# Performance work log

Hardware: AMD Instinct MI355X
Metric: run time of the kernel (lower is better)

## Reference

```python
import jax, jax.numpy as jnp
import numpy as np

B, S, D, H = 2, 2048, 1024, 16
DK = D // H

def setup_inputs() -> dict:
    key = jax.random.key(0)
    ks = jax.random.split(key, 11)
    s = 1.0 / np.sqrt(D)
    inp = {
        'q': jax.random.normal(ks[0], (B, S, D), jnp.float32),
        'k': jax.random.normal(ks[1], (B, S, D), jnp.float32),
        'v': jax.random.normal(ks[2], (B, S, D), jnp.float32),
        'mask': jnp.tril(jnp.ones((S, S), jnp.bool_))[None, None],  # [1,1,S,S] causal
        'w_q': jax.random.normal(ks[3], (D, D), jnp.float32) * s,
        'b_q': jax.random.normal(ks[4], (D,), jnp.float32) * s,
        'w_k': jax.random.normal(ks[5], (D, D), jnp.float32) * s,
        'b_k': jax.random.normal(ks[6], (D,), jnp.float32) * s,
        'w_v': jax.random.normal(ks[7], (D, D), jnp.float32) * s,
        'b_v': jax.random.normal(ks[8], (D,), jnp.float32) * s,
        'w_o': jax.random.normal(ks[9], (D, D), jnp.float32) * s,
        'b_o': jax.random.normal(ks[10], (D,), jnp.float32) * s,
    }
    return inp

def reference(q, k, v, mask, w_q, b_q, w_k, b_k, w_v, b_v, w_o, b_o):
    # Linear projections (torch Linear: x @ W^T + b)
    qh = (q @ w_q.T + b_q).reshape(B, S, H, DK).transpose(0, 2, 1, 3)  # [B,H,S,DK]
    kh = (k @ w_k.T + b_k).reshape(B, S, H, DK).transpose(0, 2, 1, 3)
    vh = (v @ w_v.T + b_v).reshape(B, S, H, DK).transpose(0, 2, 1, 3)
    scores = jnp.einsum('bhqd,bhkd->bhqk', qh, kh) / jnp.sqrt(jnp.float32(DK))
    scores = jnp.where(mask, scores, jnp.float32(-jnp.inf))
    attn = jax.nn.softmax(scores, axis=-1)  # dropout p=0.0 -> identity
    out = jnp.einsum('bhqk,bhkd->bhqd', attn, vh)
    out = out.transpose(0, 2, 1, 3).reshape(B, S, D)
    return out @ w_o.T + b_o
```

## Files before the change

kernel.cpp:

```cpp
#include <hip/hip_runtime.h>
#include <hip/hip_bf16.h>

typedef __bf16 bf16_t;
typedef __bf16 bf16x4 __attribute__((ext_vector_type(4)));
typedef __bf16 bf16x8 __attribute__((ext_vector_type(8)));
typedef float f32x4 __attribute__((ext_vector_type(4)));

#define B_ 2
#define S_ 2048
#define D_ 1024
#define H_ 16
#define DK_ 64
#define M_ (B_ * S_)

__device__ __forceinline__ f32x4 mfma16(bf16x8 a, bf16x8 b, f32x4 c) {
  return __builtin_amdgcn_mfma_f32_16x16x32_bf16(a, b, c, 0, 0, 0);
}

__device__ __forceinline__ void async_load16(const bf16_t* g, bf16_t* l) {
  __builtin_amdgcn_global_load_lds(
      (const __attribute__((address_space(1))) void*)g,
      (__attribute__((address_space(3))) void*)l, 16, 0, 0);
}


__global__ void cvt_all(const float* __restrict__ q, const float* __restrict__ k,
                        const float* __restrict__ v, const float* __restrict__ w0,
                        const float* __restrict__ w1, const float* __restrict__ w2,
                        const float* __restrict__ w3, bf16_t* __restrict__ qb,
                        bf16_t* __restrict__ kb, bf16_t* __restrict__ vb,
                        bf16_t* __restrict__ o0, bf16_t* __restrict__ o1,
                        bf16_t* __restrict__ o2, bf16_t* __restrict__ o3) {
  const int y = blockIdx.y;
  if (y >= 3 && blockIdx.x >= 512) return;
  const float* src;
  bf16_t* dst;
  float sc = 1.0f;
  switch (y) {
    case 0: src = q; dst = qb; break;
    case 1: src = k; dst = kb; break;
    case 2: src = v; dst = vb; break;
    case 3: src = w0; dst = o0; sc = 0.125f; break;
    case 4: src = w1; dst = o1; break;
    case 5: src = w2; dst = o2; break;
    default: src = w3; dst = o3; break;
  }
  long i = ((long)blockIdx.x * blockDim.x + threadIdx.x) * 8;
  const float4* s4 = (const float4*)(src + i);
  float4 a = s4[0], b = s4[1];
  bf16x8 o;
  o[0] = (bf16_t)(a.x * sc); o[1] = (bf16_t)(a.y * sc);
  o[2] = (bf16_t)(a.z * sc); o[3] = (bf16_t)(a.w * sc);
  o[4] = (bf16_t)(b.x * sc); o[5] = (bf16_t)(b.y * sc);
  o[6] = (bf16_t)(b.z * sc); o[7] = (bf16_t)(b.w * sc);
  *(bf16x8*)(dst + i) = o;
}


__device__ __forceinline__ int swzG(int b) {
  return b ^ (((b >> 7) & 7) << 4);
}

template <int NR>
__device__ __forceinline__ void stage_tile(const bf16_t* g, bf16_t* lds,
                                           const int* srcoff, int wave) {
#pragma unroll
  for (int rnd = 0; rnd < NR; ++rnd)
    async_load16(g + srcoff[rnd], lds + rnd * 2048 + wave * 512);
}

template <int MODE>
__device__ __forceinline__ void gemm_core8(const bf16_t* __restrict__ A,
                                           const bf16_t* __restrict__ W,
                                           const float* __restrict__ bias,
                                           float bscale, void* __restrict__ Cv,
                                           bf16_t* __restrict__ As,
                                           bf16_t* __restrict__ Bs) {
  constexpr int N = 1024, K = 1024;
  constexpr int TILE = 128 * 32;
  constexpr int NIT = K / 32;
  const int tid = threadIdx.x;
  const int wave = tid >> 6, lane = tid & 63;
  const int quad = lane >> 4, l15 = lane & 15;
  const int wm = wave >> 2, wn = wave & 3;
  const int bm = blockIdx.x * 128, bn = blockIdx.y * 128;

  f32x4 acc[4][2] = {};

  const int sb = swzG(tid * 16);
  const int srcoff = (sb >> 6) * K + ((sb & 63) >> 1);
  const bf16_t* ag = A + (long)bm * K;
  const bf16_t* bg = W + (long)bn * K;
  bf16_t* const adst = As;
  bf16_t* const bdst = Bs;

  const int xorv = ((l15 >> 1) & 7) << 4;
  const int aco = (((wm * 64 + l15) * 64 + quad * 16) ^ xorv) >> 1;
  const int bco = (((wn * 32 + l15) * 64 + quad * 16) ^ xorv) >> 1;

  async_load16(ag + srcoff, adst + wave * 512);
  async_load16(bg + srcoff, bdst + wave * 512);
  async_load16(ag + 32 + srcoff, adst + TILE + wave * 512);
  async_load16(bg + 32 + srcoff, bdst + TILE + wave * 512);

  int rb = 0, sb2 = 2;
  for (int j = 0; j < NIT; ++j) {
    if (j < NIT - 1)
      asm volatile("s_waitcnt vmcnt(2)" ::: "memory");
    else
      asm volatile("s_waitcnt vmcnt(0)" ::: "memory");
    __builtin_amdgcn_sched_barrier(0);
    __builtin_amdgcn_s_barrier();
    __builtin_amdgcn_sched_barrier(0);

    if (j + 2 < NIT) {
      const int kk2 = (j + 2) * 32;
      async_load16(ag + kk2 + srcoff, adst + sb2 * TILE + wave * 512);
      async_load16(bg + kk2 + srcoff, bdst + sb2 * TILE + wave * 512);
    }
    sb2 = (sb2 == 2) ? 0 : sb2 + 1;

    const bf16_t* Ac = As + rb * TILE;
    const bf16_t* Bc = Bs + rb * TILE;
    rb = (rb == 2) ? 0 : rb + 1;
    bf16x8 af[4], bfr[2];
#pragma unroll
    for (int i = 0; i < 4; ++i)
      af[i] = *(const bf16x8*)&Ac[aco + i * 512];
#pragma unroll
    for (int i = 0; i < 2; ++i)
      bfr[i] = *(const bf16x8*)&Bc[bco + i * 512];
    __builtin_amdgcn_s_setprio(1);
#pragma unroll
    for (int mi = 0; mi < 4; ++mi)
#pragma unroll
      for (int ni = 0; ni < 2; ++ni)
        acc[mi][ni] = mfma16(af[mi], bfr[ni], acc[mi][ni]);
    __builtin_amdgcn_s_setprio(0);
  }

#pragma unroll
  for (int mi = 0; mi < 4; ++mi) {
#pragma unroll
    for (int ni = 0; ni < 2; ++ni) {
      const int col = bn + wn * 32 + ni * 16 + l15;
      const float bsv = bias[col] * bscale;
      f32x4 v = acc[mi][ni];
      const int row0 = bm + wm * 64 + mi * 16 + quad * 4;
      if (MODE == 3) {
        float* C = (float*)Cv;
#pragma unroll
        for (int r = 0; r < 4; ++r)
          C[(long)(row0 + r) * N + col] = v[r] + bsv;
      } else if (MODE == 1) {
        bf16_t* C = (bf16_t*)Cv;
        const int hh = col >> 6, dk = col & 63;
        const int bq = row0 >> 11, s0 = row0 & 2047;
        bf16_t* base = C + (((long)bq * H_ + hh) * S_ + s0) * DK_ + dk;
#pragma unroll
        for (int r = 0; r < 4; ++r)
          base[(long)r * DK_] = (bf16_t)(v[r] + bsv);
      } else {
        bf16_t* C = (bf16_t*)Cv;
        const int hh = col >> 6, dk = col & 63;
        const int bq = row0 >> 11, s0 = row0 & 2047;
        bf16x4 pk;
#pragma unroll
        for (int r = 0; r < 4; ++r) pk[r] = (bf16_t)(v[r] + bsv);
        *(bf16x4*)(C + (((long)bq * H_ + hh) * DK_ + dk) * S_ + s0) = pk;
      }
    }
  }
}

__global__ __launch_bounds__(512) void gemm_qkv(
    const bf16_t* __restrict__ qb, const bf16_t* __restrict__ kb,
    const bf16_t* __restrict__ vb, const bf16_t* __restrict__ wq,
    const bf16_t* __restrict__ wk, const bf16_t* __restrict__ wv,
    const float* __restrict__ biq, const float* __restrict__ bik,
    const float* __restrict__ biv, bf16_t* __restrict__ Qh,
    bf16_t* __restrict__ Kh, bf16_t* __restrict__ Vt) {
  __shared__ bf16_t As[3][128 * 32];
  __shared__ bf16_t Bs[3][128 * 32];
  if (blockIdx.z == 0)
    gemm_core8<1>(qb, wq, biq, 0.125f, Qh, &As[0][0], &Bs[0][0]);
  else if (blockIdx.z == 1)
    gemm_core8<1>(kb, wk, bik, 1.0f, Kh, &As[0][0], &Bs[0][0]);
  else
    gemm_core8<2>(vb, wv, biv, 1.0f, Vt, &As[0][0], &Bs[0][0]);
}


__device__ __forceinline__ int swzG128(int b) {
  return b ^ (((b >> 7) & 7) << 4);
}

__global__ __launch_bounds__(256) void gemm_out64(
    const bf16_t* __restrict__ AO, const bf16_t* __restrict__ wo,
    const float* __restrict__ bo, float* __restrict__ out) {
  constexpr int N = 1024, K = 1024;
  constexpr int ATILE = 64 * 64, BTILE = 128 * 64;
  constexpr int NIT = K / 64;
  __shared__ bf16_t As[3][ATILE];
  __shared__ bf16_t Bs[3][BTILE];
  const int tid = threadIdx.x;
  const int wave = tid >> 6, lane = tid & 63;
  const int quad = lane >> 4, l15 = lane & 15;
  const int wm = wave >> 1, wn = wave & 1;
  const int bm = blockIdx.x * 64, bn = blockIdx.y * 128;

  f32x4 acc[2][4] = {};

  int srcoff[4];
#pragma unroll
  for (int rnd = 0; rnd < 4; ++rnd) {
    const int bb = rnd * 4096 + tid * 16;
    const int sb = swzG128(bb);
    srcoff[rnd] = (sb >> 7) * K + ((sb & 127) >> 1);
  }
  const bf16_t* ag = AO + (long)bm * K;
  const bf16_t* bg = wo + (long)bn * K;

  const int co0 = ((quad * 16) ^ ((l15 & 7) << 4)) >> 1;
  const int co1 = ((quad * 16 + 64) ^ ((l15 & 7) << 4)) >> 1;
  const int arow0 = (wm * 32 + l15) * 64;
  const int brow0 = (wn * 64 + l15) * 64;

  stage_tile<2>(ag, &As[0][0], srcoff, wave);
  stage_tile<4>(bg, &Bs[0][0], srcoff, wave);
  stage_tile<2>(ag + 64, &As[1][0], srcoff, wave);
  stage_tile<4>(bg + 64, &Bs[1][0], srcoff, wave);

  int rb = 0, sb2 = 2;
  for (int j = 0; j < NIT; ++j) {
    if (j < NIT - 1)
      asm volatile("s_waitcnt vmcnt(6)" ::: "memory");
    else
      asm volatile("s_waitcnt vmcnt(0)" ::: "memory");
    __builtin_amdgcn_sched_barrier(0);
    __builtin_amdgcn_s_barrier();
    __builtin_amdgcn_sched_barrier(0);

    if (j + 2 < NIT) {
      const int kk2 = (j + 2) * 64;
      stage_tile<2>(ag + kk2, &As[sb2][0], srcoff, wave);
      stage_tile<4>(bg + kk2, &Bs[sb2][0], srcoff, wave);
    }
    sb2 = (sb2 == 2) ? 0 : sb2 + 1;

    const bf16_t* Ac = &As[rb][0];
    const bf16_t* Bc = &Bs[rb][0];
    rb = (rb == 2) ? 0 : rb + 1;
#pragma unroll
    for (int h = 0; h < 2; ++h) {
      const int co = h ? co1 : co0;
      bf16x8 af[2], bfr[4];
#pragma unroll
      for (int i = 0; i < 2; ++i)
        af[i] = *(const bf16x8*)&Ac[arow0 + i * 1024 + co];
#pragma unroll
      for (int i = 0; i < 4; ++i)
        bfr[i] = *(const bf16x8*)&Bc[brow0 + i * 1024 + co];
      __builtin_amdgcn_s_setprio(1);
#pragma unroll
      for (int mi = 0; mi < 2; ++mi)
#pragma unroll
        for (int ni = 0; ni < 4; ++ni)
          acc[mi][ni] = mfma16(af[mi], bfr[ni], acc[mi][ni]);
      __builtin_amdgcn_s_setprio(0);
    }
  }

#pragma unroll
  for (int mi = 0; mi < 2; ++mi) {
#pragma unroll
    for (int ni = 0; ni < 4; ++ni) {
      const int col = bn + wn * 64 + ni * 16 + l15;
      const float bsv = bo[col];
      f32x4 v = acc[mi][ni];
      const int row0 = bm + wm * 32 + mi * 16 + quad * 4;
#pragma unroll
      for (int r = 0; r < 4; ++r)
        out[(long)(row0 + r) * N + col] = v[r] + bsv;
    }
  }
}


__device__ __forceinline__ int swzK(int b) {
  return b ^ (((b >> 7) & 3) << 4) ^ (((b >> 10) & 1) << 6);
}
__device__ __forceinline__ int swzV(int b) {
  return b ^ (((b >> 7) & 7) << 4);
}

template <bool MASKED>
__device__ __forceinline__ void softmax_pa(const f32x4 st[4], float& l_i,
                                           bf16x8& pa0, bf16x8& pa1,
                                           const int qcol, const int quad) {
#pragma unroll
  for (int nb = 0; nb < 4; ++nb) {
    const int kvb = quad * 8 + (nb & 1) * 4 + (nb >> 1) * 32;
#pragma unroll
    for (int r = 0; r < 4; ++r) {
      float x = st[nb][r];
      if (MASKED && (kvb + r) > qcol) x = -30000.f;
      const float pv = __expf(x);
      l_i += pv;
      const bf16_t pb = (bf16_t)pv;
      const int idx = ((nb & 1) << 2) | r;
      if (nb < 2) pa0[idx] = pb;
      else        pa1[idx] = pb;
    }
  }
}

__global__ __launch_bounds__(256, 2) void flash_attn3(
    const bf16_t* __restrict__ Qh, const bf16_t* __restrict__ Kh,
    const bf16_t* __restrict__ Vt, bf16_t* __restrict__ AO) {
  const int bid = blockIdx.x;
  const int g = bid & 31;
  const int i = bid >> 5;
  const int h = g & 15, b = g >> 4;
  const int tA = i, tB = 31 - i;
  const int tid = threadIdx.x, wave = tid >> 6, lane = tid & 63;
  const int quad = lane >> 4, l15 = lane & 15;
  const int qcol = wave * 16 + l15;
  const int prow = ((l15 >> 2) << 3) | (l15 & 3);

  __shared__ bf16_t Kls[3][64 * 64];
  __shared__ bf16_t Vls[3][64 * 64];

  const bf16_t* qhead = Qh + ((long)(b * H_ + h) * S_) * DK_;
  const bf16_t* khead = Kh + ((long)(b * H_ + h) * S_) * DK_;
  const bf16_t* vhead = Vt + ((long)(b * H_ + h) * DK_) * S_;

  int koffe[2], voffe[2], ldse[2];
#pragma unroll
  for (int c = 0; c < 2; ++c) {
    const int bb = c * 4096 + wave * 1024 + lane * 16;
    koffe[c] = swzK(bb) >> 1;
    const int vs = swzV(bb);
    voffe[c] = (vs >> 7) * S_ + ((vs & 127) >> 1);
    ldse[c] = c * 2048 + wave * 512;
  }

  int kro[4][2], vro[4][2];
#pragma unroll
  for (int nb = 0; nb < 4; ++nb) {
    const int krow = prow + (nb & 1) * 4 + (nb >> 1) * 32;
    const int vrow = nb * 16 + l15;
#pragma unroll
    for (int hh = 0; hh < 2; ++hh) {
      kro[nb][hh] = swzK(krow * 128 + quad * 16 + hh * 64) >> 1;
      vro[nb][hh] = swzV(vrow * 128 + quad * 16 + hh * 64) >> 1;
    }
  }

  const int qA = tA * 64 + wave * 16;
  const int qB = tB * 64 + wave * 16;
  const bf16_t* qpA = qhead + (long)(qA + l15) * DK_ + quad * 8;
  const bf16_t* qpB = qhead + (long)(qB + l15) * DK_ + quad * 8;
  const bf16x8 aqA0 = *(const bf16x8*)qpA;
  const bf16x8 aqA1 = *(const bf16x8*)(qpA + 32);
  const bf16x8 aqB0 = *(const bf16x8*)qpB;
  const bf16x8 aqB1 = *(const bf16x8*)(qpB + 32);

  f32x4 oA[4] = {}, oB[4] = {};
  float lA = 0.f, lB = 0.f;

#pragma unroll
  for (int c = 0; c < 2; ++c) {
    async_load16(khead + koffe[c], &Kls[0][ldse[c]]);
    async_load16(vhead + voffe[c], &Vls[0][ldse[c]]);
  }
#pragma unroll
  for (int c = 0; c < 2; ++c) {
    async_load16(khead + 64 * DK_ + koffe[c], &Kls[1][ldse[c]]);
    async_load16(vhead + 64 + voffe[c], &Vls[1][ldse[c]]);
  }

  int bi = 0;
  for (int j = 0; j <= tB; ++j) {
    if (j < tB)
      asm volatile("s_waitcnt vmcnt(4)" ::: "memory");
    else
      asm volatile("s_waitcnt vmcnt(0)" ::: "memory");
    __builtin_amdgcn_sched_barrier(0);
    __builtin_amdgcn_s_barrier();
    __builtin_amdgcn_sched_barrier(0);

    if (j + 2 <= tB) {
      const int tb2 = (bi == 0) ? 2 : (bi - 1);
      const bf16_t* kt = khead + (j + 2) * (64 * DK_);
      const bf16_t* vt = vhead + (j + 2) * 64;
#pragma unroll
      for (int c = 0; c < 2; ++c) {
        async_load16(kt + koffe[c], &Kls[tb2][ldse[c]]);
        async_load16(vt + voffe[c], &Vls[tb2][ldse[c]]);
      }
    }
    __builtin_amdgcn_sched_barrier(0);

    const bf16_t* Kc = &Kls[bi][0];
    const bf16_t* Vc = &Vls[bi][0];

    bf16x8 k0[4], k1[4];
#pragma unroll
    for (int nb = 0; nb < 4; ++nb) {
      k0[nb] = *(const bf16x8*)&Kc[kro[nb][0]];
      k1[nb] = *(const bf16x8*)&Kc[kro[nb][1]];
    }

    bf16x8 paB0, paB1, paA0, paA1;
    {
      f32x4 stB[4];
#pragma unroll
      for (int nb = 0; nb < 4; ++nb) {
        f32x4 t = {};
        t = mfma16(k0[nb], aqB0, t);
        t = mfma16(k1[nb], aqB1, t);
        stB[nb] = t;
      }
      if (j == tB)
        softmax_pa<true>(stB, lB, paB0, paB1, qcol, quad);
      else
        softmax_pa<false>(stB, lB, paB0, paB1, qcol, quad);
    }
    const bool doA = (j <= tA);
    if (doA) {
      f32x4 stA[4];
#pragma unroll
      for (int nb = 0; nb < 4; ++nb) {
        f32x4 t = {};
        t = mfma16(k0[nb], aqA0, t);
        t = mfma16(k1[nb], aqA1, t);
        stA[nb] = t;
      }
      if (j == tA)
        softmax_pa<true>(stA, lA, paA0, paA1, qcol, quad);
      else
        softmax_pa<false>(stA, lA, paA0, paA1, qcol, quad);
    }

    bf16x8 v0[4], v1[4];
#pragma unroll
    for (int nb = 0; nb < 4; ++nb) {
      v0[nb] = *(const bf16x8*)&Vc[vro[nb][0]];
      v1[nb] = *(const bf16x8*)&Vc[vro[nb][1]];
    }
#pragma unroll
    for (int nb = 0; nb < 4; ++nb) {
      oB[nb] = mfma16(paB0, v0[nb], oB[nb]);
      oB[nb] = mfma16(paB1, v1[nb], oB[nb]);
    }
    if (doA) {
#pragma unroll
      for (int nb = 0; nb < 4; ++nb) {
        oA[nb] = mfma16(paA0, v0[nb], oA[nb]);
        oA[nb] = mfma16(paA1, v1[nb], oA[nb]);
      }
    }

    bi = (bi == 2) ? 0 : bi + 1;
  }

  lA += __shfl_xor(lA, 16, 64);
  lA += __shfl_xor(lA, 32, 64);
  lB += __shfl_xor(lB, 16, 64);
  lB += __shfl_xor(lB, 32, 64);

  bf16_t* aoA = AO + (long)(b * S_ + qA + quad * 4) * D_ + h * DK_ + l15;
  bf16_t* aoB = AO + (long)(b * S_ + qB + quad * 4) * D_ + h * DK_ + l15;
#pragma unroll
  for (int r = 0; r < 4; ++r) {
    const float invA = 1.0f / __shfl(lA, quad * 4 + r, 64);
    const float invB = 1.0f / __shfl(lB, quad * 4 + r, 64);
#pragma unroll
    for (int nb = 0; nb < 4; ++nb) {
      aoA[(long)r * D_ + nb * 16] = (bf16_t)(oA[nb][r] * invA);
      aoB[(long)r * D_ + nb * 16] = (bf16_t)(oB[nb][r] * invB);
    }
  }
}


extern "C" void kernel_launch(void* const* d_in, const int* in_sizes, int n_in,
                              void* d_out, int out_size, void* d_ws, size_t ws_size,
                              hipStream_t stream) {
  const float* q = (const float*)d_in[0];
  const float* k = (const float*)d_in[1];
  const float* v = (const float*)d_in[2];
  const float* wq = (const float*)d_in[4];
  const float* bq = (const float*)d_in[5];
  const float* wk = (const float*)d_in[6];
  const float* bk = (const float*)d_in[7];
  const float* wv = (const float*)d_in[8];
  const float* bv = (const float*)d_in[9];
  const float* wo = (const float*)d_in[10];
  const float* bo = (const float*)d_in[11];
  float* out = (float*)d_out;

  char* ws = (char*)d_ws;
  const size_t MB = 1024 * 1024;
  bf16_t* Qh = (bf16_t*)(ws);
  bf16_t* Kh = (bf16_t*)(ws + 8 * MB);
  bf16_t* Vt = (bf16_t*)(ws + 16 * MB);
  bf16_t* AO = (bf16_t*)(ws + 24 * MB);
  bf16_t* qb = (bf16_t*)(ws + 32 * MB);
  bf16_t* kb = (bf16_t*)(ws + 40 * MB);
  bf16_t* vb = (bf16_t*)(ws + 48 * MB);
  bf16_t* wqb = (bf16_t*)(ws + 56 * MB);
  bf16_t* wkb = (bf16_t*)(ws + 58 * MB);
  bf16_t* wvb = (bf16_t*)(ws + 60 * MB);
  bf16_t* wob = (bf16_t*)(ws + 62 * MB);

  cvt_all<<<dim3(2048, 7, 1), 256, 0, stream>>>(q, k, v, wq, wk, wv, wo, qb, kb,
                                                vb, wqb, wkb, wvb, wob);
  gemm_qkv<<<dim3(32, 8, 3), 512, 0, stream>>>(qb, kb, vb, wqb, wkb, wvb, bq, bk,
                                               bv, Qh, Kh, Vt);
  flash_attn3<<<dim3(512, 1, 1), 256, 0, stream>>>(Qh, Kh, Vt, AO);
  gemm_out64<<<dim3(64, 8, 1), 256, 0, stream>>>(AO, wob, bo, out);
}
```

Measured before the change: 208.7 us.

## Fuse fp32-to-bf16 activation conversion into QKV projection GEMM loads

The separate pass that converted q, k and v from fp32 to bf16 is removed. The QKV GEMM now loads fp32 activation tiles into registers, converts them to bf16 and writes them to LDS itself, while the weight tiles still use async global-to-LDS loads. This drops the write and re-read of 3x8MB bf16 intermediates and shrinks the conversion kernel to weights only. In exchange, the GEMM fetches twice the A bytes, B fetches are re-read across 8 N-blocks, and the pipeline adds extra waitcnt stalls with register-staged A loads.

Result: slower. 238.7 us (+14.4%).

```diff
diff --git a/kernel.cpp b/kernel.cpp
--- a/kernel.cpp
+++ b/kernel.cpp
@@ -24,25 +24,18 @@
 }
 
 
-__global__ void cvt_all(const float* __restrict__ q, const float* __restrict__ k,
-                        const float* __restrict__ v, const float* __restrict__ w0,
-                        const float* __restrict__ w1, const float* __restrict__ w2,
-                        const float* __restrict__ w3, bf16_t* __restrict__ qb,
-                        bf16_t* __restrict__ kb, bf16_t* __restrict__ vb,
-                        bf16_t* __restrict__ o0, bf16_t* __restrict__ o1,
-                        bf16_t* __restrict__ o2, bf16_t* __restrict__ o3) {
+__global__ void cvt_w(const float* __restrict__ w0, const float* __restrict__ w1,
+                      const float* __restrict__ w2, const float* __restrict__ w3,
+                      bf16_t* __restrict__ o0, bf16_t* __restrict__ o1,
+                      bf16_t* __restrict__ o2, bf16_t* __restrict__ o3) {
   const int y = blockIdx.y;
-  if (y >= 3 && blockIdx.x >= 512) return;
   const float* src;
   bf16_t* dst;
   float sc = 1.0f;
   switch (y) {
-    case 0: src = q; dst = qb; break;
-    case 1: src = k; dst = kb; break;
-    case 2: src = v; dst = vb; break;
-    case 3: src = w0; dst = o0; sc = 0.125f; break;
-    case 4: src = w1; dst = o1; break;
-    case 5: src = w2; dst = o2; break;
+    case 0: src = w0; dst = o0; sc = 0.125f; break;
+    case 1: src = w1; dst = o1; break;
+    case 2: src = w2; dst = o2; break;
     default: src = w3; dst = o3; break;
   }
   long i = ((long)blockIdx.x * blockDim.x + threadIdx.x) * 8;
@@ -70,12 +63,12 @@
 }
 
 template <int MODE>
-__device__ __forceinline__ void gemm_core8(const bf16_t* __restrict__ A,
-                                           const bf16_t* __restrict__ W,
-                                           const float* __restrict__ bias,
-                                           float bscale, void* __restrict__ Cv,
-                                           bf16_t* __restrict__ As,
-                                           bf16_t* __restrict__ Bs) {
+__device__ __forceinline__ void gemm_core8f(const float* __restrict__ A,
+                                            const bf16_t* __restrict__ W,
+                                            const float* __restrict__ bias,
+                                            float bscale, void* __restrict__ Cv,
+                                            bf16_t* __restrict__ As,
+                                            bf16_t* __restrict__ Bs) {
   constexpr int N = 1024, K = 1024;
   constexpr int TILE = 128 * 32;
   constexpr int NIT = K / 32;
@@ -87,38 +80,58 @@
 
   f32x4 acc[4][2] = {};
 
-  const int sb = swzG(tid * 16);
-  const int srcoff = (sb >> 6) * K + ((sb & 63) >> 1);
-  const bf16_t* ag = A + (long)bm * K;
+  const int sbB = swzG(tid * 16);
+  const int bsrcoff = (sbB >> 6) * K + ((sbB & 63) >> 1);
   const bf16_t* bg = W + (long)bn * K;
-  bf16_t* const adst = As;
-  bf16_t* const bdst = Bs;
+
+  const int arow = tid >> 2;
+  const int acolf = (tid & 3) * 8;
+  const int awr = swzG(tid * 16) >> 1;
+  const float* agf = A + (long)(bm + arow) * K + acolf;
+
+  float4 aA_, aB_;
+  auto issueA = [&](int t) {
+    const float4* p = (const float4*)(agf + t * 32);
+    aA_ = p[0];
+    aB_ = p[1];
+  };
+  auto mathWriteA = [&](bf16_t* dstbuf) {
+    bf16x8 y;
+    y[0] = (bf16_t)aA_.x; y[1] = (bf16_t)aA_.y;
+    y[2] = (bf16_t)aA_.z; y[3] = (bf16_t)aA_.w;
+    y[4] = (bf16_t)aB_.x; y[5] = (bf16_t)aB_.y;
+    y[6] = (bf16_t)aB_.z; y[7] = (bf16_t)aB_.w;
+    *(bf16x8*)(dstbuf + awr) = y;
+  };
 
   const int xorv = ((l15 >> 1) & 7) << 4;
   const int aco = (((wm * 64 + l15) * 64 + quad * 16) ^ xorv) >> 1;
   const int bco = (((wn * 32 + l15) * 64 + quad * 16) ^ xorv) >> 1;
 
-  async_load16(ag + srcoff, adst + wave * 512);
-  async_load16(bg + srcoff, bdst + wave * 512);
-  async_load16(ag + 32 + srcoff, adst + TILE + wave * 512);
-  async_load16(bg + 32 + srcoff, bdst + TILE + wave * 512);
+  issueA(0);
+  async_load16(bg + bsrcoff, Bs + wave * 512);
+  mathWriteA(As);
+  issueA(1);
+  async_load16(bg + 32 + bsrcoff, Bs + TILE + wave * 512);
 
   int rb = 0, sb2 = 2;
   for (int j = 0; j < NIT; ++j) {
+    if (j + 1 < NIT) mathWriteA(As + ((j + 1) % 3) * TILE);
     if (j < NIT - 1)
-      asm volatile("s_waitcnt vmcnt(2)" ::: "memory");
+      asm volatile("s_waitcnt vmcnt(1)" ::: "memory");
     else
       asm volatile("s_waitcnt vmcnt(0)" ::: "memory");
+    asm volatile("s_waitcnt lgkmcnt(0)" ::: "memory");
     __builtin_amdgcn_sched_barrier(0);
     __builtin_amdgcn_s_barrier();
     __builtin_amdgcn_sched_barrier(0);
 
     if (j + 2 < NIT) {
-      const int kk2 = (j + 2) * 32;
-      async_load16(ag + kk2 + srcoff, adst + sb2 * TILE + wave * 512);
-      async_load16(bg + kk2 + srcoff, bdst + sb2 * TILE + wave * 512);
+      issueA(j + 2);
+      async_load16(bg + (j + 2) * 32 + bsrcoff, Bs + sb2 * TILE + wave * 512);
     }
     sb2 = (sb2 == 2) ? 0 : sb2 + 1;
+    __builtin_amdgcn_sched_barrier(0);
 
     const bf16_t* Ac = As + rb * TILE;
     const bf16_t* Bc = Bs + rb * TILE;
@@ -147,12 +160,7 @@
       const float bsv = bias[col] * bscale;
       f32x4 v = acc[mi][ni];
       const int row0 = bm + wm * 64 + mi * 16 + quad * 4;
-      if (MODE == 3) {
-        float* C = (float*)Cv;
-#pragma unroll
-        for (int r = 0; r < 4; ++r)
-          C[(long)(row0 + r) * N + col] = v[r] + bsv;
-      } else if (MODE == 1) {
+      if (MODE == 1) {
         bf16_t* C = (bf16_t*)Cv;
         const int hh = col >> 6, dk = col & 63;
         const int bq = row0 >> 11, s0 = row0 & 2047;
@@ -174,8 +182,8 @@
 }
 
 __global__ __launch_bounds__(512) void gemm_qkv(
-    const bf16_t* __restrict__ qb, const bf16_t* __restrict__ kb,
-    const bf16_t* __restrict__ vb, const bf16_t* __restrict__ wq,
+    const float* __restrict__ qf, const float* __restrict__ kf,
+    const float* __restrict__ vf, const bf16_t* __restrict__ wq,
     const bf16_t* __restrict__ wk, const bf16_t* __restrict__ wv,
     const float* __restrict__ biq, const float* __restrict__ bik,
     const float* __restrict__ biv, bf16_t* __restrict__ Qh,
@@ -183,11 +191,11 @@
   __shared__ bf16_t As[3][128 * 32];
   __shared__ bf16_t Bs[3][128 * 32];
   if (blockIdx.z == 0)
-    gemm_core8<1>(qb, wq, biq, 0.125f, Qh, &As[0][0], &Bs[0][0]);
+    gemm_core8f<1>(qf, wq, biq, 0.125f, Qh, &As[0][0], &Bs[0][0]);
   else if (blockIdx.z == 1)
-    gemm_core8<1>(kb, wk, bik, 1.0f, Kh, &As[0][0], &Bs[0][0]);
+    gemm_core8f<1>(kf, wk, bik, 1.0f, Kh, &As[0][0], &Bs[0][0]);
   else
-    gemm_core8<2>(vb, wv, biv, 1.0f, Vt, &As[0][0], &Bs[0][0]);
+    gemm_core8f<2>(vf, wv, biv, 1.0f, Vt, &As[0][0], &Bs[0][0]);
 }
 
 
@@ -507,17 +515,13 @@
   bf16_t* Kh = (bf16_t*)(ws + 8 * MB);
   bf16_t* Vt = (bf16_t*)(ws + 16 * MB);
   bf16_t* AO = (bf16_t*)(ws + 24 * MB);
-  bf16_t* qb = (bf16_t*)(ws + 32 * MB);
-  bf16_t* kb = (bf16_t*)(ws + 40 * MB);
-  bf16_t* vb = (bf16_t*)(ws + 48 * MB);
   bf16_t* wqb = (bf16_t*)(ws + 56 * MB);
   bf16_t* wkb = (bf16_t*)(ws + 58 * MB);
   bf16_t* wvb = (bf16_t*)(ws + 60 * MB);
   bf16_t* wob = (bf16_t*)(ws + 62 * MB);
 
-  cvt_all<<<dim3(2048, 7, 1), 256, 0, stream>>>(q, k, v, wq, wk, wv, wo, qb, kb,
-                                                vb, wqb, wkb, wvb, wob);
-  gemm_qkv<<<dim3(32, 8, 3), 512, 0, stream>>>(qb, kb, vb, wqb, wkb, wvb, bq, bk,
+  cvt_w<<<dim3(512, 4, 1), 256, 0, stream>>>(wq, wk, wv, wo, wqb, wkb, wvb, wob);
+  gemm_qkv<<<dim3(32, 8, 3), 512, 0, stream>>>(q, k, v, wqb, wkb, wvb, bq, bk,
                                                bv, Qh, Kh, Vt);
   flash_attn3<<<dim3(512, 1, 1), 256, 0, stream>>>(Qh, Kh, Vt, AO);
   gemm_out64<<<dim3(64, 8, 1), 256, 0, stream>>>(AO, wob, bo, out);
```
